# Optimization experiments

Measured on AMD Instinct MI355X. Metric: run time of the kernel, lower is better.

Reference implementation:

```python
import jax, jax.numpy as jnp
import numpy as np

EPS = 1e-10

def _normalized_gradient(x):
    # x: [B, C, H, W]. Central diff in interior, one-sided diff at boundaries.
    g_x = jnp.concatenate([
        x[:, :, 1:2, :] - x[:, :, 0:1, :],       # forward diff at top row
        x[:, :, 2:, :] - x[:, :, :-2, :],        # central diff interior
        x[:, :, -1:, :] - x[:, :, -2:-1, :],     # backward diff at bottom row
    ], axis=2)
    g_y = jnp.concatenate([
        x[:, :, :, 1:2] - x[:, :, :, 0:1],
        x[:, :, :, 2:] - x[:, :, :, :-2],
        x[:, :, :, -1:] - x[:, :, :, -2:-1],
    ], axis=3)
    g = jnp.stack([g_x, g_y], axis=-1)           # [B, C, H, W, 2]
    norm = jnp.sqrt(jnp.sum(g * g, axis=-1, keepdims=True) + EPS)
    return g / norm

def setup_inputs() -> dict:
    key = jax.random.key(0)
    k0, k1 = jax.random.split(key)
    shape = (64, 1, 512, 512)
    I0 = jax.random.normal(k0, shape, dtype=jnp.float32)
    I1 = jax.random.normal(k1, shape, dtype=jnp.float32)
    return {"I0": I0, "I1": I1}

def reference(I0, I1):
    g0 = _normalized_gradient(I0)
    g1 = _normalized_gradient(I1)
    # per-pixel dot product of the two unit gradient vectors
    dot = jnp.sum(g0 * g1, axis=-1)              # [B, C, H, W]
    return 1.0 - jnp.mean(dot * dot)
```

## Files before the change

### kernel.cpp

```cpp
#include <hip/hip_runtime.h>


#define HH 512
#define WW 512
#define NGF_EPS 1e-10f

__device__ __forceinline__ float get(const float4& v, int i) {
    return i == 0 ? v.x : i == 1 ? v.y : i == 2 ? v.z : v.w;
}

__global__ __launch_bounds__(256, 4) void ngf_partial(const float* __restrict__ I0,
                                                      const float* __restrict__ I1,
                                                      float* __restrict__ partials) {
    const int t    = blockIdx.x * 256 + threadIdx.x;
    const int w4   = t & 127;
    const int rest = t >> 7;
    const int h4   = rest & 127;
    const int img  = rest >> 7;
    const int w    = w4 << 2;
    const int h0   = h4 << 2;

    const float* p0 = I0 + (size_t)img * (HH * WW);
    const float* p1 = I1 + (size_t)img * (HH * WW);

    int roff[6];
#pragma unroll
    for (int j = 0; j < 6; ++j) {
        int r = h0 - 1 + j;
        r = r < 0 ? 0 : (r > HH - 1 ? HH - 1 : r);
        roff[j] = r * WW;
    }
    const int wl = (w > 0) ? w - 1 : 0;
    const int wq = (w + 4 < WW) ? w + 4 : WW - 1;

    float4 A0[6], A1[6];
#pragma unroll
    for (int j = 0; j < 6; ++j) {
        A0[j] = *(const float4*)(p0 + roff[j] + w);
        A1[j] = *(const float4*)(p1 + roff[j] + w);
    }
    float l0[4], q0[4], l1[4], q1[4];
#pragma unroll
    for (int r = 0; r < 4; ++r) {
        l0[r] = p0[roff[r + 1] + wl];
        q0[r] = p0[roff[r + 1] + wq];
        l1[r] = p1[roff[r + 1] + wl];
        q1[r] = p1[roff[r + 1] + wq];
    }

    float s = 0.f;
#pragma unroll
    for (int r = 0; r < 4; ++r) {
#pragma unroll
        for (int i = 0; i < 4; ++i) {
            const float gx0 = get(A0[r + 2], i) - get(A0[r], i);
            const float gx1 = get(A1[r + 2], i) - get(A1[r], i);
            const float am0 = (i == 0) ? l0[r] : get(A0[r + 1], i - 1);
            const float ap0 = (i == 3) ? q0[r] : get(A0[r + 1], i + 1);
            const float am1 = (i == 0) ? l1[r] : get(A1[r + 1], i - 1);
            const float ap1 = (i == 3) ? q1[r] : get(A1[r + 1], i + 1);
            const float gy0 = ap0 - am0;
            const float gy1 = ap1 - am1;
            const float n0 = gx0 * gx0 + gy0 * gy0 + NGF_EPS;
            const float n1 = gx1 * gx1 + gy1 * gy1 + NGF_EPS;
            const float cross = gx0 * gx1 + gy0 * gy1;
            s += cross * cross * __frcp_rn(n0 * n1);
        }
    }

#pragma unroll
    for (int off = 32; off > 0; off >>= 1) s += __shfl_down(s, off, 64);

    __shared__ float lds[4];
    const int wave = threadIdx.x >> 6;
    const int lane = threadIdx.x & 63;
    if (lane == 0) lds[wave] = s;
    __syncthreads();
    if (threadIdx.x == 0)
        partials[blockIdx.x] = lds[0] + lds[1] + lds[2] + lds[3];
}

__global__ __launch_bounds__(1024) void ngf_finalize(const float4* __restrict__ partials,
                                                     float inv_n,
                                                     float* __restrict__ out) {
    const float4 v = partials[threadIdx.x];
    float s = v.x + v.y + v.z + v.w;
#pragma unroll
    for (int off = 32; off > 0; off >>= 1) s += __shfl_down(s, off, 64);

    __shared__ float lds[16];
    const int wave = threadIdx.x >> 6;
    const int lane = threadIdx.x & 63;
    if (lane == 0) lds[wave] = s;
    __syncthreads();
    if (threadIdx.x == 0) {
        float tot = 0.f;
#pragma unroll
        for (int i = 0; i < 16; ++i) tot += lds[i];
        out[0] = 1.0f - tot * inv_n;
    }
}

extern "C" void kernel_launch(void* const* d_in, const int* in_sizes, int n_in,
                              void* d_out, int out_size, void* d_ws, size_t ws_size,
                              hipStream_t stream) {
    const float* I0 = (const float*)d_in[0];
    const float* I1 = (const float*)d_in[1];
    float* partials = (float*)d_ws;

    const int N        = in_sizes[0];
    const int nthreads = N / 16;
    const int nblocks  = nthreads / 256;

    ngf_partial<<<nblocks, 256, 0, stream>>>(I0, I1, partials);
    ngf_finalize<<<1, 1024, 0, stream>>>((const float4*)partials,
                                         1.0f / (float)N, (float*)d_out);
}
```

Baseline: 144.9 us.

## Stage row strips in LDS via direct global-to-LDS loads

```diff
diff --git a/kernel.cpp b/kernel.cpp
--- a/kernel.cpp
+++ b/kernel.cpp
@@ -4,6 +4,11 @@
 #define HH 512
 #define WW 512
 #define NGF_EPS 1e-10f
+#define RROWS 8
+#define WROWS (RROWS + 2)
+
+typedef const __attribute__((address_space(1))) void global_cv;
+typedef __attribute__((address_space(3))) void lds_v;
 
 __device__ __forceinline__ float get(const float4& v, int i) {
     return i == 0 ? v.x : i == 1 ? v.y : i == 2 ? v.z : v.w;
@@ -12,53 +17,62 @@
 __global__ __launch_bounds__(256, 4) void ngf_partial(const float* __restrict__ I0,
                                                       const float* __restrict__ I1,
                                                       float* __restrict__ partials) {
-    const int t    = blockIdx.x * 256 + threadIdx.x;
-    const int w4   = t & 127;
-    const int rest = t >> 7;
-    const int h4   = rest & 127;
-    const int img  = rest >> 7;
-    const int w    = w4 << 2;
-    const int h0   = h4 << 2;
+    __shared__ float smem[2 * WROWS * WW];
+
+    const int tid  = threadIdx.x;
+    const int img  = blockIdx.x >> 6;
+    const int rb   = blockIdx.x & 63;
+    const int h0   = rb * RROWS;
+    const int wave = tid >> 6;
+    const int lane = tid & 63;
 
     const float* p0 = I0 + (size_t)img * (HH * WW);
     const float* p1 = I1 + (size_t)img * (HH * WW);
 
-    int roff[6];
 #pragma unroll
-    for (int j = 0; j < 6; ++j) {
-        int r = h0 - 1 + j;
-        r = r < 0 ? 0 : (r > HH - 1 ? HH - 1 : r);
-        roff[j] = r * WW;
+    for (int it = 0; it < 10; ++it) {
+        const int q  = wave + it * 4;
+        const int x  = q & 1;
+        const int jm = q >> 1;
+        const int m  = (jm >= WROWS) ? 1 : 0;
+        const int j  = jm - m * WROWS;
+        int grow = h0 - 1 + j;
+        grow = grow < 0 ? 0 : (grow > HH - 1 ? HH - 1 : grow);
+        const float* src = (m ? p1 : p0) + grow * WW + x * 256 + lane * 4;
+        float* dst = smem + (m * WROWS + j) * WW + x * 256;
+        __builtin_amdgcn_global_load_lds((global_cv*)src, (lds_v*)dst, 16, 0, 0);
     }
-    const int wl = (w > 0) ? w - 1 : 0;
-    const int wq = (w + 4 < WW) ? w + 4 : WW - 1;
-
-    float4 A0[6], A1[6];
-#pragma unroll
-    for (int j = 0; j < 6; ++j) {
-        A0[j] = *(const float4*)(p0 + roff[j] + w);
-        A1[j] = *(const float4*)(p1 + roff[j] + w);
-    }
-    float l0[4], q0[4], l1[4], q1[4];
-#pragma unroll
-    for (int r = 0; r < 4; ++r) {
-        l0[r] = p0[roff[r + 1] + wl];
-        q0[r] = p0[roff[r + 1] + wq];
-        l1[r] = p1[roff[r + 1] + wl];
-        q1[r] = p1[roff[r + 1] + wq];
-    }
+    __syncthreads();
 
     float s = 0.f;
 #pragma unroll
-    for (int r = 0; r < 4; ++r) {
+    for (int k = 0; k < 4; ++k) {
+        const int g = k * 256 + tid;
+        const int r = g >> 7;
+        const int w = (g & 127) << 2;
+        const float* s0 = smem + r * WW;
+        const float* s1 = smem + (WROWS + r) * WW;
+
+        const float4 u0 = *(const float4*)(s0 + w);
+        const float4 c0 = *(const float4*)(s0 + WW + w);
+        const float4 d0 = *(const float4*)(s0 + 2 * WW + w);
+        const float  l0 = (w > 0)      ? s0[WW + w - 1] : c0.x;
+        const float  q0 = (w < WW - 4) ? s0[WW + w + 4] : c0.w;
+
+        const float4 u1 = *(const float4*)(s1 + w);
+        const float4 c1 = *(const float4*)(s1 + WW + w);
+        const float4 d1 = *(const float4*)(s1 + 2 * WW + w);
+        const float  l1 = (w > 0)      ? s1[WW + w - 1] : c1.x;
+        const float  q1 = (w < WW - 4) ? s1[WW + w + 4] : c1.w;
+
 #pragma unroll
         for (int i = 0; i < 4; ++i) {
-            const float gx0 = get(A0[r + 2], i) - get(A0[r], i);
-            const float gx1 = get(A1[r + 2], i) - get(A1[r], i);
-            const float am0 = (i == 0) ? l0[r] : get(A0[r + 1], i - 1);
-            const float ap0 = (i == 3) ? q0[r] : get(A0[r + 1], i + 1);
-            const float am1 = (i == 0) ? l1[r] : get(A1[r + 1], i - 1);
-            const float ap1 = (i == 3) ? q1[r] : get(A1[r + 1], i + 1);
+            const float gx0 = get(d0, i) - get(u0, i);
+            const float gx1 = get(d1, i) - get(u1, i);
+            const float am0 = (i == 0) ? l0 : get(c0, i - 1);
+            const float ap0 = (i == 3) ? q0 : get(c0, i + 1);
+            const float am1 = (i == 0) ? l1 : get(c1, i - 1);
+            const float ap1 = (i == 3) ? q1 : get(c1, i + 1);
             const float gy0 = ap0 - am0;
             const float gy1 = ap1 - am1;
             const float n0 = gx0 * gx0 + gy0 * gy0 + NGF_EPS;
@@ -71,13 +85,11 @@
 #pragma unroll
     for (int off = 32; off > 0; off >>= 1) s += __shfl_down(s, off, 64);
 
-    __shared__ float lds[4];
-    const int wave = threadIdx.x >> 6;
-    const int lane = threadIdx.x & 63;
-    if (lane == 0) lds[wave] = s;
+    __shared__ float red[4];
+    if (lane == 0) red[wave] = s;
     __syncthreads();
-    if (threadIdx.x == 0)
-        partials[blockIdx.x] = lds[0] + lds[1] + lds[2] + lds[3];
+    if (tid == 0)
+        partials[blockIdx.x] = red[0] + red[1] + red[2] + red[3];
 }
 
 __global__ __launch_bounds__(1024) void ngf_finalize(const float4* __restrict__ partials,
@@ -108,9 +120,8 @@
     const float* I1 = (const float*)d_in[1];
     float* partials = (float*)d_ws;
 
-    const int N        = in_sizes[0];
-    const int nthreads = N / 16;
-    const int nblocks  = nthreads / 256;
+    const int N = in_sizes[0];
+    const int nblocks = 64 * (HH / RROWS);
 
     ngf_partial<<<nblocks, 256, 0, stream>>>(I0, I1, partials);
     ngf_finalize<<<1, 1024, 0, stream>>>((const float4*)partials,
```

Result: no change. 142.3 us (-1.8%).

## Stream rows per wavefront with sliding window and lane shuffles for halos

Applied to the files above, without the earlier changes.

```diff
diff --git a/kernel.cpp b/kernel.cpp
--- a/kernel.cpp
+++ b/kernel.cpp
@@ -4,91 +4,89 @@
 #define HH 512
 #define WW 512
 #define NGF_EPS 1e-10f
+#define RPT 16
 
-__device__ __forceinline__ float get(const float4& v, int i) {
-    return i == 0 ? v.x : i == 1 ? v.y : i == 2 ? v.z : v.w;
-}
+__device__ __forceinline__ float rcp_fast(float x) { return __builtin_amdgcn_rcpf(x); }
 
-__global__ __launch_bounds__(256, 4) void ngf_partial(const float* __restrict__ I0,
-                                                      const float* __restrict__ I1,
-                                                      float* __restrict__ partials) {
-    const int t    = blockIdx.x * 256 + threadIdx.x;
-    const int w4   = t & 127;
-    const int rest = t >> 7;
-    const int h4   = rest & 127;
-    const int img  = rest >> 7;
-    const int w    = w4 << 2;
-    const int h0   = h4 << 2;
+__global__ __launch_bounds__(256) void ngf_partial(const float* __restrict__ I0,
+                                                   const float* __restrict__ I1,
+                                                   float* __restrict__ partials) {
+    const int tid  = threadIdx.x;
+    const int wv   = tid >> 6;
+    const int lane = tid & 63;
+    const int gw   = blockIdx.x * 4 + wv;
+    const int img  = gw >> 5;
+    const int ck   = gw & 31;
+    const int h0   = ck * RPT;
 
-    const float* p0 = I0 + (size_t)img * (HH * WW);
-    const float* p1 = I1 + (size_t)img * (HH * WW);
+    const float* p0 = I0 + (size_t)img * (HH * WW) + lane * 8;
+    const float* p1 = I1 + (size_t)img * (HH * WW) + lane * 8;
 
-    int roff[6];
-#pragma unroll
-    for (int j = 0; j < 6; ++j) {
-        int r = h0 - 1 + j;
-        r = r < 0 ? 0 : (r > HH - 1 ? HH - 1 : r);
-        roff[j] = r * WW;
-    }
-    const int wl = (w > 0) ? w - 1 : 0;
-    const int wq = (w + 4 < WW) ? w + 4 : WW - 1;
-
-    float4 A0[6], A1[6];
-#pragma unroll
-    for (int j = 0; j < 6; ++j) {
-        A0[j] = *(const float4*)(p0 + roff[j] + w);
-        A1[j] = *(const float4*)(p1 + roff[j] + w);
-    }
-    float l0[4], q0[4], l1[4], q1[4];
-#pragma unroll
-    for (int r = 0; r < 4; ++r) {
-        l0[r] = p0[roff[r + 1] + wl];
-        q0[r] = p0[roff[r + 1] + wq];
-        l1[r] = p1[roff[r + 1] + wl];
-        q1[r] = p1[roff[r + 1] + wq];
+    float4 u0a, u0b, u1a, u1b, c0a, c0b, c1a, c1b, n0a, n0b, n1a, n1b;
+    {
+        const int ru = (h0 > 0) ? (h0 - 1) * WW : 0;
+        const int rc = h0 * WW;
+        const int rn = (h0 + 1) * WW;
+        u0a = *(const float4*)(p0 + ru);     u0b = *(const float4*)(p0 + ru + 4);
+        u1a = *(const float4*)(p1 + ru);     u1b = *(const float4*)(p1 + ru + 4);
+        c0a = *(const float4*)(p0 + rc);     c0b = *(const float4*)(p0 + rc + 4);
+        c1a = *(const float4*)(p1 + rc);     c1b = *(const float4*)(p1 + rc + 4);
+        n0a = *(const float4*)(p0 + rn);     n0b = *(const float4*)(p0 + rn + 4);
+        n1a = *(const float4*)(p1 + rn);     n1b = *(const float4*)(p1 + rn + 4);
     }
 
     float s = 0.f;
 #pragma unroll
-    for (int r = 0; r < 4; ++r) {
+    for (int i = 0; i < RPT; ++i) {
+        const int h  = h0 + i;
+        const int hm = (h + 2 < HH) ? h + 2 : HH - 1;
+        const int rm = hm * WW;
+        const float4 m0a = *(const float4*)(p0 + rm);
+        const float4 m0b = *(const float4*)(p0 + rm + 4);
+        const float4 m1a = *(const float4*)(p1 + rm);
+        const float4 m1b = *(const float4*)(p1 + rm + 4);
+
+        float L0 = __shfl_up(c0b.w, 1, 64);   if (lane == 0)  L0 = c0a.x;
+        float R0 = __shfl_down(c0a.x, 1, 64); if (lane == 63) R0 = c0b.w;
+        float L1 = __shfl_up(c1b.w, 1, 64);   if (lane == 0)  L1 = c1a.x;
+        float R1 = __shfl_down(c1a.x, 1, 64); if (lane == 63) R1 = c1b.w;
+
+        const float a0[10] = {L0, c0a.x, c0a.y, c0a.z, c0a.w,
+                                  c0b.x, c0b.y, c0b.z, c0b.w, R0};
+        const float a1[10] = {L1, c1a.x, c1a.y, c1a.z, c1a.w,
+                                  c1b.x, c1b.y, c1b.z, c1b.w, R1};
+        const float gx0[8] = {n0a.x - u0a.x, n0a.y - u0a.y, n0a.z - u0a.z, n0a.w - u0a.w,
+                              n0b.x - u0b.x, n0b.y - u0b.y, n0b.z - u0b.z, n0b.w - u0b.w};
+        const float gx1[8] = {n1a.x - u1a.x, n1a.y - u1a.y, n1a.z - u1a.z, n1a.w - u1a.w,
+                              n1b.x - u1b.x, n1b.y - u1b.y, n1b.z - u1b.z, n1b.w - u1b.w};
 #pragma unroll
-        for (int i = 0; i < 4; ++i) {
-            const float gx0 = get(A0[r + 2], i) - get(A0[r], i);
-            const float gx1 = get(A1[r + 2], i) - get(A1[r], i);
-            const float am0 = (i == 0) ? l0[r] : get(A0[r + 1], i - 1);
-            const float ap0 = (i == 3) ? q0[r] : get(A0[r + 1], i + 1);
-            const float am1 = (i == 0) ? l1[r] : get(A1[r + 1], i - 1);
-            const float ap1 = (i == 3) ? q1[r] : get(A1[r + 1], i + 1);
-            const float gy0 = ap0 - am0;
-            const float gy1 = ap1 - am1;
-            const float n0 = gx0 * gx0 + gy0 * gy0 + NGF_EPS;
-            const float n1 = gx1 * gx1 + gy1 * gy1 + NGF_EPS;
-            const float cross = gx0 * gx1 + gy0 * gy1;
-            s += cross * cross * __frcp_rn(n0 * n1);
+        for (int j = 0; j < 8; ++j) {
+            const float gy0 = a0[j + 2] - a0[j];
+            const float gy1 = a1[j + 2] - a1[j];
+            const float q0  = gx0[j] * gx0[j] + gy0 * gy0 + NGF_EPS;
+            const float q1  = gx1[j] * gx1[j] + gy1 * gy1 + NGF_EPS;
+            const float cr  = gx0[j] * gx1[j] + gy0 * gy1;
+            s += cr * cr * rcp_fast(q0 * q1);
         }
+        u0a = c0a; u0b = c0b; u1a = c1a; u1b = c1b;
+        c0a = n0a; c0b = n0b; c1a = n1a; c1b = n1b;
+        n0a = m0a; n0b = m0b; n1a = m1a; n1b = m1b;
     }
 
 #pragma unroll
     for (int off = 32; off > 0; off >>= 1) s += __shfl_down(s, off, 64);
-
-    __shared__ float lds[4];
-    const int wave = threadIdx.x >> 6;
-    const int lane = threadIdx.x & 63;
-    if (lane == 0) lds[wave] = s;
-    __syncthreads();
-    if (threadIdx.x == 0)
-        partials[blockIdx.x] = lds[0] + lds[1] + lds[2] + lds[3];
+    if (lane == 0) partials[gw] = s;
 }
 
-__global__ __launch_bounds__(1024) void ngf_finalize(const float4* __restrict__ partials,
-                                                     float inv_n,
-                                                     float* __restrict__ out) {
+__global__ __launch_bounds__(512) void ngf_finalize(const float4* __restrict__ partials,
+                                                    float inv_n,
+                                                    float* __restrict__ out) {
     const float4 v = partials[threadIdx.x];
     float s = v.x + v.y + v.z + v.w;
 #pragma unroll
     for (int off = 32; off > 0; off >>= 1) s += __shfl_down(s, off, 64);
 
-    __shared__ float lds[16];
+    __shared__ float lds[8];
     const int wave = threadIdx.x >> 6;
     const int lane = threadIdx.x & 63;
     if (lane == 0) lds[wave] = s;
@@ -96,7 +94,7 @@
     if (threadIdx.x == 0) {
         float tot = 0.f;
 #pragma unroll
-        for (int i = 0; i < 16; ++i) tot += lds[i];
+        for (int i = 0; i < 8; ++i) tot += lds[i];
         out[0] = 1.0f - tot * inv_n;
     }
 }
@@ -108,11 +106,8 @@
     const float* I1 = (const float*)d_in[1];
     float* partials = (float*)d_ws;
 
-    const int N        = in_sizes[0];
-    const int nthreads = N / 16;
-    const int nblocks  = nthreads / 256;
-
-    ngf_partial<<<nblocks, 256, 0, stream>>>(I0, I1, partials);
-    ngf_finalize<<<1, 1024, 0, stream>>>((const float4*)partials,
-                                         1.0f / (float)N, (float*)d_out);
+    const int N = in_sizes[0];
+    ngf_partial<<<512, 256, 0, stream>>>(I0, I1, partials);
+    ngf_finalize<<<1, 512, 0, stream>>>((const float4*)partials,
+                                        1.0f / (float)N, (float*)d_out);
 }
```

Result: no change. 144.4 us (-0.4%).
